# Optimization experiments

Hardware: AMD Instinct MI355X
Metric: run time of the kernel (lower is better)

Reference implementation:

```python
import jax, jax.numpy as jnp
import numpy as np

N = 200_000          # nodes
E = 12_800_000       # directed edges (avg degree 64)
C = 5                # channels: [pos_x, pos_y, vel_x, vel_y, extra]
ACCEL_SCALE = 0.01
MAX_VEL = 0.1
MAX_POS = 1.0


def setup_inputs() -> dict:
    key = jax.random.key(0)
    k1, k2, k3 = jax.random.split(key, 3)
    x = jax.random.uniform(k1, (N, C), jnp.float32, -1.0, 1.0)
    edge_index = jax.random.randint(k2, (2, E), 0, N, dtype=jnp.int32)
    # GCNConv learned params (glorot-ish init, zero bias as in PyG)
    W = jax.random.normal(k3, (C, 2), jnp.float32) * (1.0 / np.sqrt(C))
    b = jnp.zeros((2,), jnp.float32)
    return {"x": x, "edge_index": edge_index, "W": W, "b": b, "time_steps": 1}


def _gcn_conv(x, edge_index, W, b):
    """PyG GCNConv: add self-loops, symmetric deg normalization, X @ W, scatter-sum."""
    n = x.shape[0]
    loop = jnp.arange(n, dtype=edge_index.dtype)
    src = jnp.concatenate([edge_index[0], loop])  # [E+N]
    dst = jnp.concatenate([edge_index[1], loop])
    deg = jax.ops.segment_sum(jnp.ones_like(src, x.dtype), dst, num_segments=n)  # [N]
    dinv = jnp.where(deg > 0, jax.lax.rsqrt(deg), 0.0)
    norm = dinv[src] * dinv[dst]                  # [E+N]
    h = x @ W                                     # [N, 2]
    msg = h[src] * norm[:, None]                  # gather + scale, [E+N, 2]
    out = jax.ops.segment_sum(msg, dst, num_segments=n) + b
    return out


def _step(x, edge_index, W, b):
    acc = _gcn_conv(x, edge_index, W, b) * ACCEL_SCALE        # [N, 2]
    vel = jnp.clip(x[:, 2:4] + acc, -MAX_VEL, MAX_VEL)
    pos = jnp.clip(x[:, :2] + vel, -MAX_POS, MAX_POS)
    return jnp.concatenate([pos, vel, x[:, 4:]], axis=1)


def reference(x, edge_index, W, b, time_steps):
    for _ in range(time_steps):
        x = _step(x, edge_index, W, b)
    return x
```

## Files before the change

kernel.cpp:

```cpp
#include <hip/hip_runtime.h>
#include <hip/hip_fp16.h>

constexpr float ACCEL_SCALE = 0.01f;
constexpr float MAX_VEL = 0.1f;
constexpr float MAX_POS = 1.0f;

constexpr int GSHIFT = 11;
constexpr int GSIZE  = 1 << GSHIFT;
constexpr int SCANW  = 128;
constexpr int REP    = 4;
constexpr int ANBLK  = 1024;
constexpr int DSHIFT = 4;
constexpr int ASHIFT = 5;


__global__ __launch_bounds__(256) void h_scatter_kernel(
    const int* __restrict__ src, const int* __restrict__ dst,
    int E, int NG, int chunk,
    unsigned* __restrict__ tab, unsigned* __restrict__ packed)
{
    __shared__ int cnt4[SCANW * REP];
    __shared__ int tmp[SCANW];
    __shared__ int cur[SCANW];
    int tid = threadIdx.x;
    int c = tid & (REP - 1);
    long long cs64 = (long long)blockIdx.x * chunk;
    int cs = (cs64 > E) ? E : (int)cs64;
    int ce = min(cs + chunk, E);

    for (int i = tid; i < SCANW * REP; i += 256) cnt4[i] = 0;
    __syncthreads();

    int nv = (ce - cs) >> 2;
    const int4* d4 = (const int4*)(dst + cs);
    for (int k = tid; k < nv; k += 256) {
        int4 v = d4[k];
        atomicAdd(&cnt4[((v.x >> GSHIFT) << 2) | c], 1);
        atomicAdd(&cnt4[((v.y >> GSHIFT) << 2) | c], 1);
        atomicAdd(&cnt4[((v.z >> GSHIFT) << 2) | c], 1);
        atomicAdd(&cnt4[((v.w >> GSHIFT) << 2) | c], 1);
    }
    for (int i = cs + (nv << 2) + tid; i < ce; i += 256)
        atomicAdd(&cnt4[((dst[i] >> GSHIFT) << 2) | c], 1);
    __syncthreads();

    int v = 0;
    if (tid < SCANW) {
        int b4 = tid << 2;
        v = cnt4[b4] + cnt4[b4 | 1] + cnt4[b4 | 2] + cnt4[b4 | 3];
        tmp[tid] = v;
    }
    __syncthreads();
    for (int off = 1; off < SCANW; off <<= 1) {
        int t = (tid < SCANW && tid >= off) ? tmp[tid - off] : 0;
        __syncthreads();
        if (tid < SCANW) tmp[tid] += t;
        __syncthreads();
    }
    if (tid < SCANW) {
        int base = tmp[tid] - v;
        cur[tid] = base;
        if (tid <= NG) tab[(size_t)blockIdx.x * (NG + 1) + tid] = (unsigned)base;
    }
    __syncthreads();

    const int4* s4 = (const int4*)(src + cs);
    for (int k = tid; k < nv; k += 256) {
        int4 dv = d4[k];
        int4 sv = s4[k];
        int p;
        p = atomicAdd(&cur[dv.x >> GSHIFT], 1);
        packed[cs + p] = ((unsigned)sv.x << GSHIFT) | (unsigned)(dv.x & (GSIZE - 1));
        p = atomicAdd(&cur[dv.y >> GSHIFT], 1);
        packed[cs + p] = ((unsigned)sv.y << GSHIFT) | (unsigned)(dv.y & (GSIZE - 1));
        p = atomicAdd(&cur[dv.z >> GSHIFT], 1);
        packed[cs + p] = ((unsigned)sv.z << GSHIFT) | (unsigned)(dv.z & (GSIZE - 1));
        p = atomicAdd(&cur[dv.w >> GSHIFT], 1);
        packed[cs + p] = ((unsigned)sv.w << GSHIFT) | (unsigned)(dv.w & (GSIZE - 1));
    }
    for (int i = cs + (nv << 2) + tid; i < ce; i += 256) {
        int dvv = dst[i], svv = src[i];
        int p = atomicAdd(&cur[dvv >> GSHIFT], 1);
        packed[cs + p] = ((unsigned)svv << GSHIFT) | (unsigned)(dvv & (GSIZE - 1));
    }
}

__global__ __launch_bounds__(512) void f_deg_kernel(
    const unsigned* __restrict__ packed, const unsigned* __restrict__ tab,
    int E, int NG, int chunk, int n, int splitShift, int* __restrict__ pdeg)
{
    __shared__ int cnt[GSIZE];
    int g = blockIdx.x >> splitShift;
    int s = blockIdx.x & ((1 << splitShift) - 1);
    for (int t = threadIdx.x; t < GSIZE; t += 512) cnt[t] = 0;
    __syncthreads();
    int wave = threadIdx.x >> 6, lane = threadIdx.x & 63;
    int perSplit = ANBLK >> splitShift;
    int j0 = s * perSplit, jend = j0 + perSplit;
    int j = j0 + wave;
    unsigned nt0 = 0, nt1 = 0;
    if (j < jend) { const unsigned* tr = tab + (size_t)j * (NG + 1) + g; nt0 = tr[0]; nt1 = tr[1]; }
    for (; j < jend; j += 8) {
        unsigned t0 = nt0, t1 = nt1;
        int jn = j + 8;
        if (jn < jend) { const unsigned* tr = tab + (size_t)jn * (NG + 1) + g; nt0 = tr[0]; nt1 = tr[1]; }
        long long cs64 = (long long)j * chunk;
        int cs = (cs64 > E) ? E : (int)cs64;
        for (unsigned i = t0 + lane; i < t1; i += 64)
            atomicAdd(&cnt[packed[cs + i] & (GSIZE - 1)], 1);
    }
    __syncthreads();
    size_t nb0 = (size_t)g << GSHIFT;
    for (int t = threadIdx.x; t < GSIZE; t += 512) {
        size_t node = nb0 + t;
        if (node < (size_t)n) pdeg[(size_t)s * n + node] = cnt[t];
    }
}

__global__ void node_preh_kernel(const float* __restrict__ x, const float* __restrict__ W,
                                 const int* __restrict__ pdeg, int n, int nsplit,
                                 float* __restrict__ dinv, __half2* __restrict__ hsh) {
    int i = blockIdx.x * blockDim.x + threadIdx.x;
    if (i >= n) return;
    int d = 1;
    for (int s = 0; s < nsplit; ++s) d += pdeg[(size_t)s * n + i];
    float di = rsqrtf((float)d);
    dinv[i] = di;
    const float* xr = x + (size_t)i * 5;
    float x0 = xr[0], x1 = xr[1], x2 = xr[2], x3 = xr[3], x4 = xr[4];
    float h0 = x0 * W[0] + x1 * W[2] + x2 * W[4] + x3 * W[6] + x4 * W[8];
    float h1 = x0 * W[1] + x1 * W[3] + x2 * W[5] + x3 * W[7] + x4 * W[9];
    hsh[i] = __floats2half2_rn(h0 * di, h1 * di);
}

__global__ __launch_bounds__(512) void a_acc5_kernel(
    const unsigned* __restrict__ packed, const unsigned* __restrict__ tab,
    const __half2* __restrict__ hsh, int E, int NG, int chunk, int n,
    __half2* __restrict__ psh)
{
    __shared__ __half2 acc[GSIZE];
    int g = blockIdx.x >> ASHIFT;
    int s = blockIdx.x & ((1 << ASHIFT) - 1);
    const __half2 zero = __floats2half2_rn(0.f, 0.f);
    for (int t = threadIdx.x; t < GSIZE; t += 512) acc[t] = zero;
    __syncthreads();
    int wave = threadIdx.x >> 6, lane = threadIdx.x & 63;
    const int perSplit = ANBLK >> ASHIFT;
    int j0 = s * perSplit, jend = j0 + perSplit;
    int j = j0 + wave;
    unsigned nt0 = 0, nt1 = 0;
    if (j < jend) { const unsigned* tr = tab + (size_t)j * (NG + 1) + g; nt0 = tr[0]; nt1 = tr[1]; }
    for (; j < jend; j += 8) {
        unsigned t0 = nt0, t1 = nt1;
        int jn = j + 8;
        if (jn < jend) { const unsigned* tr = tab + (size_t)jn * (NG + 1) + g; nt0 = tr[0]; nt1 = tr[1]; }
        long long cs64 = (long long)j * chunk;
        int cs = (cs64 > E) ? E : (int)cs64;
        for (unsigned i = t0 + lane; i < t1; i += 64) {
            unsigned p = packed[cs + i];
            __half2 m = hsh[p >> GSHIFT];
            unsafeAtomicAdd(&acc[p & (GSIZE - 1)], m);
        }
    }
    __syncthreads();
    size_t nb0 = (size_t)g << GSHIFT;
    for (int t = threadIdx.x; t < GSIZE; t += 512) {
        size_t node = nb0 + t;
        if (node < (size_t)n) psh[(size_t)s * n + node] = acc[t];
    }
}

__global__ void a_finalh_kernel(const float* __restrict__ x, const __half2* __restrict__ psh,
                                const float* __restrict__ W, const float* __restrict__ dinv,
                                const float* __restrict__ b, float* __restrict__ out,
                                int n, int nsplit) {
    int i = blockIdx.x * blockDim.x + threadIdx.x;
    if (i >= n) return;
    float sx = 0.f, sy = 0.f;
    for (int s = 0; s < nsplit; ++s) {
        float2 v = __half22float2(psh[(size_t)s * n + i]);
        sx += v.x; sy += v.y;
    }
    float di = dinv[i];
    const float* xr = x + (size_t)i * 5;
    float x0 = xr[0], x1 = xr[1], x2 = xr[2], x3 = xr[3], x4 = xr[4];
    float h0 = x0 * W[0] + x1 * W[2] + x2 * W[4] + x3 * W[6] + x4 * W[8];
    float h1 = x0 * W[1] + x1 * W[3] + x2 * W[5] + x3 * W[7] + x4 * W[9];
    float c0 = di * (sx + h0 * di) + b[0];
    float c1 = di * (sy + h1 * di) + b[1];
    float a0 = c0 * ACCEL_SCALE;
    float a1 = c1 * ACCEL_SCALE;
    float v0 = fminf(fmaxf(x2 + a0, -MAX_VEL), MAX_VEL);
    float v1 = fminf(fmaxf(x3 + a1, -MAX_VEL), MAX_VEL);
    float p0 = fminf(fmaxf(x0 + v0, -MAX_POS), MAX_POS);
    float p1 = fminf(fmaxf(x1 + v1, -MAX_POS), MAX_POS);
    float* o = out + (size_t)i * 5;
    o[0] = p0; o[1] = p1; o[2] = v0; o[3] = v1; o[4] = x4;
}

__global__ void fb_deg_kernel(const int* __restrict__ dst, int E, int* __restrict__ deg) {
    int tid = blockIdx.x * blockDim.x + threadIdx.x;
    int stride = gridDim.x * blockDim.x;
    for (int k = tid; k < E; k += stride) atomicAdd(&deg[dst[k]], 1);
}
__global__ void fb_scatter_kernel(const int* __restrict__ src, const int* __restrict__ dst,
                                  int E, const float* __restrict__ hs, float* __restrict__ s) {
    int tid = blockIdx.x * blockDim.x + threadIdx.x;
    int stride = gridDim.x * blockDim.x;
    const float2* h2 = (const float2*)hs;
    for (int k = tid; k < E; k += stride) {
        int sv = src[k], dv = dst[k];
        float2 m = h2[sv];
        unsafeAtomicAdd(&s[2 * dv], m.x);
        unsafeAtomicAdd(&s[2 * dv + 1], m.y);
    }
}
__global__ void fb_np_kernel(const float* __restrict__ x, const float* __restrict__ W,
                             const int* __restrict__ deg, int n,
                             float* __restrict__ dinv, float* __restrict__ hs) {
    int i = blockIdx.x * blockDim.x + threadIdx.x;
    if (i >= n) return;
    float di = rsqrtf((float)(deg[i] + 1));
    dinv[i] = di;
    const float* xr = x + (size_t)i * 5;
    float x0 = xr[0], x1 = xr[1], x2 = xr[2], x3 = xr[3], x4 = xr[4];
    float h0 = x0 * W[0] + x1 * W[2] + x2 * W[4] + x3 * W[6] + x4 * W[8];
    float h1 = x0 * W[1] + x1 * W[3] + x2 * W[5] + x3 * W[7] + x4 * W[9];
    hs[2 * i] = h0 * di;
    hs[2 * i + 1] = h1 * di;
}
__global__ void fb_finalize_kernel(const float* __restrict__ x, const float* __restrict__ s,
                                   const float* __restrict__ hs, const float* __restrict__ dinv,
                                   const float* __restrict__ b, float* __restrict__ out, int n) {
    int i = blockIdx.x * blockDim.x + threadIdx.x;
    if (i >= n) return;
    float di = dinv[i];
    const float2* s2 = (const float2*)s;
    const float2* h2 = (const float2*)hs;
    float2 sv = s2[i];
    float2 hv = h2[i];
    float c0 = di * (sv.x + hv.x) + b[0];
    float c1 = di * (sv.y + hv.y) + b[1];
    float a0 = c0 * ACCEL_SCALE, a1 = c1 * ACCEL_SCALE;
    const float* xr = x + (size_t)i * 5;
    float v0 = fminf(fmaxf(xr[2] + a0, -MAX_VEL), MAX_VEL);
    float v1 = fminf(fmaxf(xr[3] + a1, -MAX_VEL), MAX_VEL);
    float p0 = fminf(fmaxf(xr[0] + v0, -MAX_POS), MAX_POS);
    float p1 = fminf(fmaxf(xr[1] + v1, -MAX_POS), MAX_POS);
    float* o = out + (size_t)i * 5;
    o[0] = p0; o[1] = p1; o[2] = v0; o[3] = v1; o[4] = xr[4];
}

extern "C" void kernel_launch(void* const* d_in, const int* in_sizes, int n_in,
                              void* d_out, int out_size, void* d_ws, size_t ws_size,
                              hipStream_t stream) {
    const float* x    = (const float*)d_in[0];
    const int*   edge = (const int*)d_in[1];
    const float* W    = (const float*)d_in[2];
    const float* b    = (const float*)d_in[3];

    int n = in_sizes[0] / 5;
    int E = in_sizes[1] / 2;
    const int* src = edge;
    const int* dst = edge + E;

    const int BLK = 256;
    int node_blocks = (n + BLK - 1) / BLK;
    int NG = (n + GSIZE - 1) >> GSHIFT;
    int chunk = ((E + ANBLK - 1) / ANBLK + 3) & ~3;
    const int dsplit = 1 << DSHIFT;
    const int asplit = 1 << ASHIFT;
    bool geomOK = (NG >= 1) && (NG + 1 <= SCANW) && (n <= (1 << 21)) && (E >= 8);

    size_t wTab = (size_t)ANBLK * (NG + 1);
    size_t needW = (size_t)E + wTab + (size_t)dsplit * n + (size_t)asplit * n
                 + (size_t)n + (size_t)n;

    if (geomOK && ws_size >= needW * 4) {
        unsigned* packed = (unsigned*)d_ws;
        unsigned* tab    = packed + E;
        int*      pdeg   = (int*)(tab + wTab);
        __half2*  psh    = (__half2*)(pdeg + (size_t)dsplit * n);
        float*    dinv   = (float*)(psh + (size_t)asplit * n);
        __half2*  hsh    = (__half2*)(dinv + n);

        h_scatter_kernel<<<ANBLK, 256, 0, stream>>>(src, dst, E, NG, chunk, tab, packed);
        f_deg_kernel<<<NG << DSHIFT, 512, 0, stream>>>(packed, tab, E, NG, chunk, n,
                                                       DSHIFT, pdeg);
        node_preh_kernel<<<node_blocks, BLK, 0, stream>>>(x, W, pdeg, n, dsplit, dinv, hsh);
        a_acc5_kernel<<<NG << ASHIFT, 512, 0, stream>>>(packed, tab, hsh, E, NG, chunk, n,
                                                        psh);
        a_finalh_kernel<<<node_blocks, BLK, 0, stream>>>(x, psh, W, dinv, b,
                                                         (float*)d_out, n, asplit);
        return;
    }

    {
        float* dinv = (float*)d_ws;
        float* hs   = dinv + n;
        float* s    = hs + 2 * (size_t)n;
        int*   deg  = (int*)(s + 2 * (size_t)n);
        hipMemsetAsync(deg, 0, (size_t)n * sizeof(int), stream);
        hipMemsetAsync(s,   0, (size_t)n * 2 * sizeof(float), stream);
        fb_deg_kernel<<<4096, BLK, 0, stream>>>(dst, E, deg);
        fb_np_kernel<<<node_blocks, BLK, 0, stream>>>(x, W, deg, n, dinv, hs);
        fb_scatter_kernel<<<4096, BLK, 0, stream>>>(src, dst, E, hs, s);
        fb_finalize_kernel<<<node_blocks, BLK, 0, stream>>>(x, s, hs, dinv, b, (float*)d_out, n);
    }
}
```

Baseline: 174.4 us.

## Bucket edges into padded interleaved per-group segments with sentinel fill

Adds a new primary path whose bucketing kernel gives each (block, node-group) segment four interleaved sub-streams, each with its own LDS cursor. Slots are padded to the longest sub-stream and empty slots are filled with a sentinel, using an output buffer about 1.5x the chunk size. The aim is to cut shared-atomic contention in the scatter pass, since each cursor is shared by only a quarter of the threads. The degree and accumulate kernels now skip sentinels, and psh reuses the pdeg memory to shrink the workspace. The cost is extra padded reads and writes, per-element branches, and a workspace layout that relies on the 1.5x padding being enough.

```diff
diff --git a/kernel.cpp b/kernel.cpp
--- a/kernel.cpp
+++ b/kernel.cpp
@@ -12,6 +12,208 @@
 constexpr int ANBLK  = 1024;
 constexpr int DSHIFT = 4;
 constexpr int ASHIFT = 5;
+constexpr unsigned SENT = 0xFFFFFFFFu;
+
+
+__global__ __launch_bounds__(256) void i_scatter_kernel(
+    const int* __restrict__ src, const int* __restrict__ dst,
+    int E, int NG, int chunk, int ochunk,
+    unsigned* __restrict__ tab, unsigned* __restrict__ packed)
+{
+    __shared__ int cnt4[SCANW * REP];
+    __shared__ int cur4[SCANW * REP];
+    __shared__ int mx[SCANW];
+    __shared__ int tmp[SCANW];
+    __shared__ int bb[SCANW];
+    int tid = threadIdx.x;
+    int c = tid & (REP - 1);
+    long long cs64 = (long long)blockIdx.x * chunk;
+    int cs = (cs64 > E) ? E : (int)cs64;
+    int ce = min(cs + chunk, E);
+    size_t ob = (size_t)blockIdx.x * ochunk;
+
+    for (int i = tid; i < SCANW * REP; i += 256) { cnt4[i] = 0; cur4[i] = 0; }
+    __syncthreads();
+
+    int nv = (ce - cs) >> 2;
+    const int4* d4 = (const int4*)(dst + cs);
+    for (int k = tid; k < nv; k += 256) {
+        int4 v = d4[k];
+        atomicAdd(&cnt4[((v.x >> GSHIFT) << 2) | c], 1);
+        atomicAdd(&cnt4[((v.y >> GSHIFT) << 2) | c], 1);
+        atomicAdd(&cnt4[((v.z >> GSHIFT) << 2) | c], 1);
+        atomicAdd(&cnt4[((v.w >> GSHIFT) << 2) | c], 1);
+    }
+    for (int i = cs + (nv << 2) + tid; i < ce; i += 256)
+        atomicAdd(&cnt4[((dst[i] >> GSHIFT) << 2) | c], 1);
+    __syncthreads();
+
+    int seglen = 0;
+    if (tid < SCANW) {
+        int b4 = tid << 2;
+        int m = max(max(cnt4[b4], cnt4[b4 | 1]), max(cnt4[b4 | 2], cnt4[b4 | 3]));
+        mx[tid] = m;
+        seglen = m << 2;
+        tmp[tid] = seglen;
+    }
+    __syncthreads();
+    for (int off = 1; off < SCANW; off <<= 1) {
+        int t = (tid < SCANW && tid >= off) ? tmp[tid - off] : 0;
+        __syncthreads();
+        if (tid < SCANW) tmp[tid] += t;
+        __syncthreads();
+    }
+    if (tid < SCANW) {
+        int base = tmp[tid] - seglen;
+        bb[tid] = base;
+        if (tid <= NG) tab[(size_t)blockIdx.x * (NG + 1) + tid] = (unsigned)base;
+    }
+    __syncthreads();
+
+    for (int i = tid; i < (NG << 2); i += 256) {
+        int b = i >> 2, cc = i & 3;
+        int base = bb[b], m = mx[b];
+        for (int r = cnt4[i]; r < m; ++r)
+            packed[ob + base + (r << 2) + cc] = SENT;
+    }
+    __syncthreads();
+
+    const int4* s4 = (const int4*)(src + cs);
+    for (int k = tid; k < nv; k += 256) {
+        int4 dv = d4[k];
+        int4 sv = s4[k];
+        int b, p;
+        b = dv.x >> GSHIFT; p = atomicAdd(&cur4[(b << 2) | c], 1);
+        packed[ob + bb[b] + (p << 2) + c] = ((unsigned)sv.x << GSHIFT) | (unsigned)(dv.x & (GSIZE - 1));
+        b = dv.y >> GSHIFT; p = atomicAdd(&cur4[(b << 2) | c], 1);
+        packed[ob + bb[b] + (p << 2) + c] = ((unsigned)sv.y << GSHIFT) | (unsigned)(dv.y & (GSIZE - 1));
+        b = dv.z >> GSHIFT; p = atomicAdd(&cur4[(b << 2) | c], 1);
+        packed[ob + bb[b] + (p << 2) + c] = ((unsigned)sv.z << GSHIFT) | (unsigned)(dv.z & (GSIZE - 1));
+        b = dv.w >> GSHIFT; p = atomicAdd(&cur4[(b << 2) | c], 1);
+        packed[ob + bb[b] + (p << 2) + c] = ((unsigned)sv.w << GSHIFT) | (unsigned)(dv.w & (GSIZE - 1));
+    }
+    for (int i = cs + (nv << 2) + tid; i < ce; i += 256) {
+        int dd = dst[i], ss = src[i];
+        int b = dd >> GSHIFT;
+        int p = atomicAdd(&cur4[(b << 2) | c], 1);
+        packed[ob + bb[b] + (p << 2) + c] = ((unsigned)ss << GSHIFT) | (unsigned)(dd & (GSIZE - 1));
+    }
+}
+
+__global__ __launch_bounds__(512) void i_deg_kernel(
+    const unsigned* __restrict__ packed, const unsigned* __restrict__ tab,
+    int NG, int ochunk, int n, int* __restrict__ pdeg)
+{
+    __shared__ int cnt[GSIZE];
+    int g = blockIdx.x >> DSHIFT;
+    int s = blockIdx.x & ((1 << DSHIFT) - 1);
+    for (int t = threadIdx.x; t < GSIZE; t += 512) cnt[t] = 0;
+    __syncthreads();
+    int wave = threadIdx.x >> 6, lane = threadIdx.x & 63;
+    const int perSplit = ANBLK >> DSHIFT;
+    int j0 = s * perSplit, jend = j0 + perSplit;
+    int j = j0 + wave;
+    unsigned nt0 = 0, nt1 = 0;
+    if (j < jend) { const unsigned* tr = tab + (size_t)j * (NG + 1) + g; nt0 = tr[0]; nt1 = tr[1]; }
+    for (; j < jend; j += 8) {
+        unsigned t0 = nt0, t1 = nt1;
+        int jn = j + 8;
+        if (jn < jend) { const unsigned* tr = tab + (size_t)jn * (NG + 1) + g; nt0 = tr[0]; nt1 = tr[1]; }
+        size_t ob = (size_t)j * ochunk;
+        for (unsigned i = t0 + lane; i < t1; i += 64) {
+            unsigned p = packed[ob + i];
+            if (p != SENT) atomicAdd(&cnt[p & (GSIZE - 1)], 1);
+        }
+    }
+    __syncthreads();
+    size_t nb0 = (size_t)g << GSHIFT;
+    for (int t = threadIdx.x; t < GSIZE; t += 512) {
+        size_t node = nb0 + t;
+        if (node < (size_t)n) pdeg[(size_t)s * n + node] = cnt[t];
+    }
+}
+
+__global__ void node_preh_kernel(const float* __restrict__ x, const float* __restrict__ W,
+                                 const int* __restrict__ pdeg, int n, int nsplit,
+                                 float* __restrict__ dinv, __half2* __restrict__ hsh) {
+    int i = blockIdx.x * blockDim.x + threadIdx.x;
+    if (i >= n) return;
+    int d = 1;
+    for (int s = 0; s < nsplit; ++s) d += pdeg[(size_t)s * n + i];
+    float di = rsqrtf((float)d);
+    dinv[i] = di;
+    const float* xr = x + (size_t)i * 5;
+    float x0 = xr[0], x1 = xr[1], x2 = xr[2], x3 = xr[3], x4 = xr[4];
+    float h0 = x0 * W[0] + x1 * W[2] + x2 * W[4] + x3 * W[6] + x4 * W[8];
+    float h1 = x0 * W[1] + x1 * W[3] + x2 * W[5] + x3 * W[7] + x4 * W[9];
+    hsh[i] = __floats2half2_rn(h0 * di, h1 * di);
+}
+
+__global__ __launch_bounds__(512) void i_acc_kernel(
+    const unsigned* __restrict__ packed, const unsigned* __restrict__ tab,
+    const __half2* __restrict__ hsh, int NG, int ochunk, int n,
+    __half2* __restrict__ psh)
+{
+    __shared__ __half2 acc[GSIZE];
+    int g = blockIdx.x >> ASHIFT;
+    int s = blockIdx.x & ((1 << ASHIFT) - 1);
+    const __half2 zero = __floats2half2_rn(0.f, 0.f);
+    for (int t = threadIdx.x; t < GSIZE; t += 512) acc[t] = zero;
+    __syncthreads();
+    int wave = threadIdx.x >> 6, lane = threadIdx.x & 63;
+    const int perSplit = ANBLK >> ASHIFT;
+    int j0 = s * perSplit, jend = j0 + perSplit;
+    int j = j0 + wave;
+    unsigned nt0 = 0, nt1 = 0;
+    if (j < jend) { const unsigned* tr = tab + (size_t)j * (NG + 1) + g; nt0 = tr[0]; nt1 = tr[1]; }
+    for (; j < jend; j += 8) {
+        unsigned t0 = nt0, t1 = nt1;
+        int jn = j + 8;
+        if (jn < jend) { const unsigned* tr = tab + (size_t)jn * (NG + 1) + g; nt0 = tr[0]; nt1 = tr[1]; }
+        size_t ob = (size_t)j * ochunk;
+        for (unsigned i = t0 + lane; i < t1; i += 64) {
+            unsigned p = packed[ob + i];
+            if (p != SENT) {
+                __half2 m = hsh[p >> GSHIFT];
+                unsafeAtomicAdd(&acc[p & (GSIZE - 1)], m);
+            }
+        }
+    }
+    __syncthreads();
+    size_t nb0 = (size_t)g << GSHIFT;
+    for (int t = threadIdx.x; t < GSIZE; t += 512) {
+        size_t node = nb0 + t;
+        if (node < (size_t)n) psh[(size_t)s * n + node] = acc[t];
+    }
+}
+
+__global__ void a_finalh_kernel(const float* __restrict__ x, const __half2* __restrict__ psh,
+                                const float* __restrict__ W, const float* __restrict__ dinv,
+                                const float* __restrict__ b, float* __restrict__ out,
+                                int n, int nsplit) {
+    int i = blockIdx.x * blockDim.x + threadIdx.x;
+    if (i >= n) return;
+    float sx = 0.f, sy = 0.f;
+    for (int s = 0; s < nsplit; ++s) {
+        float2 v = __half22float2(psh[(size_t)s * n + i]);
+        sx += v.x; sy += v.y;
+    }
+    float di = dinv[i];
+    const float* xr = x + (size_t)i * 5;
+    float x0 = xr[0], x1 = xr[1], x2 = xr[2], x3 = xr[3], x4 = xr[4];
+    float h0 = x0 * W[0] + x1 * W[2] + x2 * W[4] + x3 * W[6] + x4 * W[8];
+    float h1 = x0 * W[1] + x1 * W[3] + x2 * W[5] + x3 * W[7] + x4 * W[9];
+    float c0 = di * (sx + h0 * di) + b[0];
+    float c1 = di * (sy + h1 * di) + b[1];
+    float a0 = c0 * ACCEL_SCALE;
+    float a1 = c1 * ACCEL_SCALE;
+    float v0 = fminf(fmaxf(x2 + a0, -MAX_VEL), MAX_VEL);
+    float v1 = fminf(fmaxf(x3 + a1, -MAX_VEL), MAX_VEL);
+    float p0 = fminf(fmaxf(x0 + v0, -MAX_POS), MAX_POS);
+    float p1 = fminf(fmaxf(x1 + v1, -MAX_POS), MAX_POS);
+    float* o = out + (size_t)i * 5;
+    o[0] = p0; o[1] = p1; o[2] = v0; o[3] = v1; o[4] = x4;
+}
 
 
 __global__ __launch_bounds__(256) void h_scatter_kernel(
@@ -115,22 +317,6 @@
         size_t node = nb0 + t;
         if (node < (size_t)n) pdeg[(size_t)s * n + node] = cnt[t];
     }
-}
-
-__global__ void node_preh_kernel(const float* __restrict__ x, const float* __restrict__ W,
-                                 const int* __restrict__ pdeg, int n, int nsplit,
-                                 float* __restrict__ dinv, __half2* __restrict__ hsh) {
-    int i = blockIdx.x * blockDim.x + threadIdx.x;
-    if (i >= n) return;
-    int d = 1;
-    for (int s = 0; s < nsplit; ++s) d += pdeg[(size_t)s * n + i];
-    float di = rsqrtf((float)d);
-    dinv[i] = di;
-    const float* xr = x + (size_t)i * 5;
-    float x0 = xr[0], x1 = xr[1], x2 = xr[2], x3 = xr[3], x4 = xr[4];
-    float h0 = x0 * W[0] + x1 * W[2] + x2 * W[4] + x3 * W[6] + x4 * W[8];
-    float h1 = x0 * W[1] + x1 * W[3] + x2 * W[5] + x3 * W[7] + x4 * W[9];
-    hsh[i] = __floats2half2_rn(h0 * di, h1 * di);
 }
 
 __global__ __launch_bounds__(512) void a_acc5_kernel(
@@ -168,34 +354,6 @@
         size_t node = nb0 + t;
         if (node < (size_t)n) psh[(size_t)s * n + node] = acc[t];
     }
-}
-
-__global__ void a_finalh_kernel(const float* __restrict__ x, const __half2* __restrict__ psh,
-                                const float* __restrict__ W, const float* __restrict__ dinv,
-                                const float* __restrict__ b, float* __restrict__ out,
-                                int n, int nsplit) {
-    int i = blockIdx.x * blockDim.x + threadIdx.x;
-    if (i >= n) return;
-    float sx = 0.f, sy = 0.f;
-    for (int s = 0; s < nsplit; ++s) {
-        float2 v = __half22float2(psh[(size_t)s * n + i]);
-        sx += v.x; sy += v.y;
-    }
-    float di = dinv[i];
-    const float* xr = x + (size_t)i * 5;
-    float x0 = xr[0], x1 = xr[1], x2 = xr[2], x3 = xr[3], x4 = xr[4];
-    float h0 = x0 * W[0] + x1 * W[2] + x2 * W[4] + x3 * W[6] + x4 * W[8];
-    float h1 = x0 * W[1] + x1 * W[3] + x2 * W[5] + x3 * W[7] + x4 * W[9];
-    float c0 = di * (sx + h0 * di) + b[0];
-    float c1 = di * (sy + h1 * di) + b[1];
-    float a0 = c0 * ACCEL_SCALE;
-    float a1 = c1 * ACCEL_SCALE;
-    float v0 = fminf(fmaxf(x2 + a0, -MAX_VEL), MAX_VEL);
-    float v1 = fminf(fmaxf(x3 + a1, -MAX_VEL), MAX_VEL);
-    float p0 = fminf(fmaxf(x0 + v0, -MAX_POS), MAX_POS);
-    float p1 = fminf(fmaxf(x1 + v1, -MAX_POS), MAX_POS);
-    float* o = out + (size_t)i * 5;
-    o[0] = p0; o[1] = p1; o[2] = v0; o[3] = v1; o[4] = x4;
 }
 
 __global__ void fb_deg_kernel(const int* __restrict__ dst, int E, int* __restrict__ deg) {
@@ -268,31 +426,57 @@
     int node_blocks = (n + BLK - 1) / BLK;
     int NG = (n + GSIZE - 1) >> GSHIFT;
     int chunk = ((E + ANBLK - 1) / ANBLK + 3) & ~3;
+    int ochunk = ((chunk + (chunk >> 1)) + 3) & ~3;
     const int dsplit = 1 << DSHIFT;
     const int asplit = 1 << ASHIFT;
     bool geomOK = (NG >= 1) && (NG + 1 <= SCANW) && (n <= (1 << 21)) && (E >= 8);
 
     size_t wTab = (size_t)ANBLK * (NG + 1);
-    size_t needW = (size_t)E + wTab + (size_t)dsplit * n + (size_t)asplit * n
-                 + (size_t)n + (size_t)n;
-
-    if (geomOK && ws_size >= needW * 4) {
-        unsigned* packed = (unsigned*)d_ws;
-        unsigned* tab    = packed + E;
-        int*      pdeg   = (int*)(tab + wTab);
-        __half2*  psh    = (__half2*)(pdeg + (size_t)dsplit * n);
-        float*    dinv   = (float*)(psh + (size_t)asplit * n);
-        __half2*  hsh    = (__half2*)(dinv + n);
-
-        h_scatter_kernel<<<ANBLK, 256, 0, stream>>>(src, dst, E, NG, chunk, tab, packed);
-        f_deg_kernel<<<NG << DSHIFT, 512, 0, stream>>>(packed, tab, E, NG, chunk, n,
-                                                       DSHIFT, pdeg);
-        node_preh_kernel<<<node_blocks, BLK, 0, stream>>>(x, W, pdeg, n, dsplit, dinv, hsh);
-        a_acc5_kernel<<<NG << ASHIFT, 512, 0, stream>>>(packed, tab, hsh, E, NG, chunk, n,
-                                                        psh);
-        a_finalh_kernel<<<node_blocks, BLK, 0, stream>>>(x, psh, W, dinv, b,
-                                                         (float*)d_out, n, asplit);
-        return;
+
+    {
+        size_t needI = (size_t)ANBLK * ochunk + wTab + (size_t)asplit * n
+                     + (size_t)n + (size_t)n;
+        if (geomOK && ws_size >= needI * 4) {
+            unsigned* packed = (unsigned*)d_ws;
+            unsigned* tab    = packed + (size_t)ANBLK * ochunk;
+            int*      region = (int*)(tab + wTab);
+            int*      pdeg   = region;
+            __half2*  psh    = (__half2*)region;
+            float*    dinv   = (float*)(region + (size_t)asplit * n);
+            __half2*  hsh    = (__half2*)(dinv + n);
+
+            i_scatter_kernel<<<ANBLK, 256, 0, stream>>>(src, dst, E, NG, chunk, ochunk,
+                                                        tab, packed);
+            i_deg_kernel<<<NG << DSHIFT, 512, 0, stream>>>(packed, tab, NG, ochunk, n, pdeg);
+            node_preh_kernel<<<node_blocks, BLK, 0, stream>>>(x, W, pdeg, n, dsplit, dinv, hsh);
+            i_acc_kernel<<<NG << ASHIFT, 512, 0, stream>>>(packed, tab, hsh, NG, ochunk, n, psh);
+            a_finalh_kernel<<<node_blocks, BLK, 0, stream>>>(x, psh, W, dinv, b,
+                                                             (float*)d_out, n, asplit);
+            return;
+        }
+    }
+
+    {
+        size_t needF = (size_t)E + wTab + (size_t)dsplit * n + (size_t)asplit * n
+                     + (size_t)n + (size_t)n;
+        if (geomOK && ws_size >= needF * 4) {
+            unsigned* packed = (unsigned*)d_ws;
+            unsigned* tab    = packed + E;
+            int*      pdeg   = (int*)(tab + wTab);
+            __half2*  psh    = (__half2*)(pdeg + (size_t)dsplit * n);
+            float*    dinv   = (float*)(psh + (size_t)asplit * n);
+            __half2*  hsh    = (__half2*)(dinv + n);
+
+            h_scatter_kernel<<<ANBLK, 256, 0, stream>>>(src, dst, E, NG, chunk, tab, packed);
+            f_deg_kernel<<<NG << DSHIFT, 512, 0, stream>>>(packed, tab, E, NG, chunk, n,
+                                                           DSHIFT, pdeg);
+            node_preh_kernel<<<node_blocks, BLK, 0, stream>>>(x, W, pdeg, n, dsplit, dinv, hsh);
+            a_acc5_kernel<<<NG << ASHIFT, 512, 0, stream>>>(packed, tab, hsh, E, NG, chunk, n,
+                                                            psh);
+            a_finalh_kernel<<<node_blocks, BLK, 0, stream>>>(x, psh, W, dinv, b,
+                                                             (float*)d_out, n, asplit);
+            return;
+        }
     }
 
     {
```

New measurement: 193.5 us. 1.11x slower.
